# Optimization experiments

Measured on AMD Instinct MI355X. Metric: run time of the kernel, lower is better.

Reference implementation:

```python
import jax, jax.numpy as jnp
import numpy as np

D_C, D_K, D_T = 1024, 1024, 1024
N_KB = 65536
BATCH = 4096
ALPHA_C, ALPHA_K, ALPHA_T = 1.0, 0.5, 0.25


def setup_inputs() -> dict:
    key = jax.random.key(0)
    k1, k2, k3 = jax.random.split(key, 3)
    C = jax.random.normal(k1, (BATCH, D_C), dtype=jnp.float32)
    K = jax.random.normal(k2, (BATCH, D_K), dtype=jnp.float32)
    tie_kb = jax.random.normal(k3, (N_KB, D_T), dtype=jnp.float32)
    # Frozen Q: zero-initialized then identity on the top-left min(D_C, D_T) block.
    Q_weight = jnp.zeros((D_T, D_C), dtype=jnp.float32)
    d = min(D_C, D_T)
    Q_weight = Q_weight.at[:d, :d].set(jnp.eye(d, dtype=jnp.float32))
    return {
        "C": C,
        "K": K,
        "tie_kb": tie_kb,
        "Q_weight": Q_weight,
        "temperature": 1.0,
        "top_k": 32,
    }


def _retrieve_tie_batched(q, kb, top_k, temperature):
    """Batched version of the per-row retrieve_tie: cdist -> top-k nearest ->
    softmax(-dist/temperature) weighted sum of KB rows.
    q: [n, D_T], kb: [N_kb, D_T] -> [n, D_T]
    """
    q_sq = jnp.sum(q * q, axis=-1, keepdims=True)            # [n, 1]
    kb_sq = jnp.sum(kb * kb, axis=-1)                        # [N_kb]
    # Squared Euclidean distances via GEMM (same math as torch.cdist p=2)
    d2 = jnp.maximum(q_sq + kb_sq[None, :] - 2.0 * (q @ kb.T), 0.0)  # [n, N_kb]
    dist = jnp.sqrt(d2)
    neg_top, idx = jax.lax.top_k(-dist, top_k)               # top_k smallest dists
    w = jax.nn.softmax(neg_top / temperature, axis=-1)       # [n, top_k]
    sel = kb[idx]                                            # [n, top_k, D_T]
    return jnp.einsum('nk,nkd->nd', w, sel)


def reference(C, K, tie_kb, Q_weight, temperature, top_k):
    q = C @ Q_weight.T                                       # [n, D_T]
    T = _retrieve_tie_batched(q, tie_kb, top_k, temperature)  # [n, D_T]
    fused = jnp.concatenate([ALPHA_C * C, ALPHA_K * K, ALPHA_T * T], axis=1)
    return jax.nn.silu(fused)
```

## Files before the change

kernel.cpp:

```cpp
#include <hip/hip_runtime.h>
#include <stdint.h>

#define D_DIM   1024
#define NKB     65536
#define BATCH   4096
#define TOPK    32
#define NCHUNKS 16
#define CHUNK   4096
#define MT      128
#define NT      128
#define BKK     64
#define RB      16
#define RB_P    17

typedef float  floatx4 __attribute__((ext_vector_type(4)));
typedef __bf16 bf16x8  __attribute__((ext_vector_type(8)));

__device__ __forceinline__ uint16_t f2bf(float f) {
  union { float f; uint32_t i; } v; v.f = f;
  return (uint16_t)((v.i + 0x7fffu + ((v.i >> 16) & 1u)) >> 16);
}
__device__ __forceinline__ float silu_f(float x) { return x / (1.f + __expf(-x)); }

__device__ __forceinline__ void gl_lds16(const uint16_t* g, uint16_t* l) {
  __builtin_amdgcn_global_load_lds((const __attribute__((address_space(1))) void*)g,
                                   (__attribute__((address_space(3))) void*)l,
                                   16, 0, 0);
}

__global__ void convert_norms_kernel(const float* __restrict__ KB,
                                     const float* __restrict__ C,
                                     uint16_t* __restrict__ KBb,
                                     uint16_t* __restrict__ Cb,
                                     float* __restrict__ kbsq,
                                     float* __restrict__ qsq) {
  int wid  = (blockIdx.x * blockDim.x + threadIdx.x) >> 6;
  int lane = threadIdx.x & 63;
  if (wid >= NKB + BATCH) return;
  const float* src; uint16_t* dst;
  if (wid < NKB) { src = KB + (size_t)wid * D_DIM; dst = KBb + (size_t)wid * D_DIM; }
  else { src = C + (size_t)(wid - NKB) * D_DIM; dst = Cb + (size_t)(wid - NKB) * D_DIM; }

  const float4* p = (const float4*)src;
  uint4* q = (uint4*)dst;
  float s = 0.f;
  float4 f[4];
#pragma unroll
  for (int h = 0; h < 4; ++h) f[h] = p[lane * 4 + h];
  uint32_t ob[8];
#pragma unroll
  for (int h = 0; h < 4; ++h) {
    float vv[4] = {f[h].x, f[h].y, f[h].z, f[h].w};
#pragma unroll
    for (int e = 0; e < 4; ++e) s += vv[e] * vv[e];
    ob[h * 2]     = (uint32_t)f2bf(vv[0]) | ((uint32_t)f2bf(vv[1]) << 16);
    ob[h * 2 + 1] = (uint32_t)f2bf(vv[2]) | ((uint32_t)f2bf(vv[3]) << 16);
  }
  q[lane * 2]     = (uint4){ob[0], ob[1], ob[2], ob[3]};
  q[lane * 2 + 1] = (uint4){ob[4], ob[5], ob[6], ob[7]};
#pragma unroll
  for (int off = 32; off > 0; off >>= 1) s += __shfl_xor(s, off);
  if (lane == 0) { if (wid < NKB) kbsq[wid] = s; else qsq[wid - NKB] = s; }
}

__launch_bounds__(256, 2)
__global__ void dist_topk_kernel(const uint16_t* __restrict__ Cb,
                                 const uint16_t* __restrict__ KBb,
                                 const float* __restrict__ kbsq,
                                 const float* __restrict__ qsq,
                                 float* __restrict__ cand_d,
                                 int*   __restrict__ cand_i) {
  __shared__ __align__(16) uint16_t As[MT * BKK];
  __shared__ __align__(16) uint16_t Bs[NT * BKK];
  __shared__ float    rbd[MT * RB_P];
  __shared__ uint16_t rbi[MT * RB_P];
  __shared__ int      rbcnt[MT];
  __shared__ float    thr[MT];
  __shared__ float    qsq_l[MT];
  __shared__ int      s_any;

  const int t = threadIdx.x;
  const int w = t >> 6, lane = t & 63;
  const int lm = lane & 15, lq = lane >> 4;
  const int wr = w >> 1, wc = w & 1;
  const int row0 = blockIdx.x * MT;
  const int col0 = blockIdx.y * CHUNK;

  float tv[TOPK]; int ti[TOPK];
#pragma unroll
  for (int k = 0; k < TOPK; ++k) { tv[k] = __builtin_inff(); ti[k] = 0; }

  auto drain_rb = [&](int tt) {
    int n = rbcnt[tt]; if (n > RB) n = RB;
    for (int e = 0; e < n; ++e) {
      float d = rbd[tt * RB_P + e];
      int  iv = rbi[tt * RB_P + e];
      if (d < tv[TOPK - 1]) {
#pragma unroll
        for (int p = TOPK - 1; p >= 1; --p) {
          bool lt_prev = d < tv[p - 1];
          bool lt_here = d < tv[p];
          float nv = lt_prev ? tv[p - 1] : (lt_here ? d : tv[p]);
          int   ni = lt_prev ? ti[p - 1] : (lt_here ? iv : ti[p]);
          tv[p] = nv; ti[p] = ni;
        }
        if (d < tv[0]) { tv[0] = d; ti[0] = iv; }
      }
    }
    rbcnt[tt] = 0;
    thr[tt] = tv[TOPK - 1];
  };

  if (t < MT) { thr[t] = __builtin_inff(); rbcnt[t] = 0; qsq_l[t] = qsq[row0 + t]; }
  if (t == 0) s_any = 0;
  __syncthreads();

  bool pending = false;

  for (int ct = 0; ct < CHUNK / NT; ++ct) {
    const int cb = col0 + ct * NT;
    floatx4 acc[4][4];
#pragma unroll
    for (int i = 0; i < 4; ++i)
#pragma unroll
      for (int j = 0; j < 4; ++j) acc[i][j] = (floatx4){0.f, 0.f, 0.f, 0.f};

    for (int k0 = 0; k0 < D_DIM; k0 += BKK) {
      __syncthreads();
#pragma unroll
      for (int is = 0; is < 4; ++is) {
        int c = is * 256 + t;
        int row = c >> 3, kp = c & 7;
        int kps = kp ^ (row & 7);
        gl_lds16(Cb + (size_t)(row0 + row) * D_DIM + k0 + kps * 8,
                 &As[(is * 256 + (w << 6)) * 8]);
      }
#pragma unroll
      for (int is = 0; is < 4; ++is) {
        int c = is * 256 + t;
        int row = c >> 3, kp = c & 7;
        int kps = kp ^ (row & 7);
        gl_lds16(KBb + (size_t)(cb + row) * D_DIM + k0 + kps * 8,
                 &Bs[(is * 256 + (w << 6)) * 8]);
      }
      if (k0 == 0 && pending) {
        if (t < MT) drain_rb(t);
        pending = false;
      }
      __syncthreads();
#pragma unroll
      for (int kk = 0; kk < 2; ++kk) {
        bf16x8 af[4], bf[4];
#pragma unroll
        for (int i = 0; i < 4; ++i) {
          int r = (wr << 6) + (i << 4) + lm;
          int p = (kk * 4 + lq) ^ (r & 7);
          af[i] = *(const bf16x8*)&As[r * BKK + p * 8];
        }
#pragma unroll
        for (int j = 0; j < 4; ++j) {
          int r = (wc << 6) + (j << 4) + lm;
          int p = (kk * 4 + lq) ^ (r & 7);
          bf[j] = *(const bf16x8*)&Bs[r * BKK + p * 8];
        }
#pragma unroll
        for (int i = 0; i < 4; ++i)
#pragma unroll
          for (int j = 0; j < 4; ++j)
            acc[i][j] = __builtin_amdgcn_mfma_f32_16x16x32_bf16(af[i], bf[j], acc[i][j], 0, 0, 0);
      }
    }

    float kbc[4];
#pragma unroll
    for (int j = 0; j < 4; ++j) kbc[j] = kbsq[cb + (wc << 6) + (j << 4) + lm];

    uint64_t pend = 0;
#pragma unroll
    for (int i = 0; i < 4; ++i) {
#pragma unroll
      for (int rg = 0; rg < 4; ++rg) {
        int rl = (wr << 6) + (i << 4) + (lq << 2) + rg;
        float qv = qsq_l[rl];
        float th = thr[rl];
#pragma unroll
        for (int j = 0; j < 4; ++j) {
          float d2 = fmaf(-2.f, acc[i][j][rg], qv + kbc[j]);
          if (d2 < th) {
            int slot = atomicAdd(&rbcnt[rl], 1);
            if (slot < RB) {
              rbd[rl * RB_P + slot] = d2;
              rbi[rl * RB_P + slot] = (uint16_t)(cb + (wc << 6) + (j << 4) + lm);
            } else pend |= 1ull << ((i << 4) | (rg << 2) | j);
          }
        }
      }
    }
    if (pend) s_any = 1;
    __syncthreads();

    if (s_any) {
      while (true) {
        if (t < MT) drain_rb(t);
        if (t == 0) s_any = 0;
        __syncthreads();
        uint64_t np = 0;
#pragma unroll
        for (int i = 0; i < 4; ++i) {
#pragma unroll
          for (int rg = 0; rg < 4; ++rg) {
            int rl = (wr << 6) + (i << 4) + (lq << 2) + rg;
#pragma unroll
            for (int j = 0; j < 4; ++j) {
              const int v = (i << 4) | (rg << 2) | j;
              if (pend & (1ull << v)) {
                float d2 = fmaf(-2.f, acc[i][j][rg], qsq_l[rl] + kbc[j]);
                if (d2 < thr[rl]) {
                  int slot = atomicAdd(&rbcnt[rl], 1);
                  if (slot < RB) {
                    rbd[rl * RB_P + slot] = d2;
                    rbi[rl * RB_P + slot] = (uint16_t)(cb + (wc << 6) + (j << 4) + lm);
                  } else np |= 1ull << v;
                }
              }
            }
          }
        }
        pend = np;
        if (pend) s_any = 1;
        __syncthreads();
        if (!s_any) break;
      }
    } else {
      pending = true;
    }
  }

  if (pending) {
    if (t < MT) drain_rb(t);
  }

  if (t < MT) {
    size_t base = ((size_t)(row0 + t) * NCHUNKS + blockIdx.y) * TOPK;
#pragma unroll
    for (int k = 0; k < TOPK; ++k) {
      cand_d[base + k] = tv[k];
      cand_i[base + k] = ti[k];
    }
  }
}

__global__ void merge_kernel(const float* __restrict__ Cm,
                             const float* __restrict__ Km,
                             const float* __restrict__ KB,
                             const float* __restrict__ cand_d,
                             const int*   __restrict__ cand_i,
                             float* __restrict__ out) {
  __shared__ float sel_d[4][TOPK];
  __shared__ int   sel_i[4][TOPK];
  __shared__ float wgt[4][TOPK];
  int w = threadIdx.x >> 6, lane = threadIdx.x & 63;
  int R = blockIdx.x * 4 + w;

  float v[8]; int ix[8];
#pragma unroll
  for (int s = 0; s < 8; ++s) {
    v[s]  = cand_d[(size_t)R * (NCHUNKS * TOPK) + s * 64 + lane];
    ix[s] = cand_i[(size_t)R * (NCHUNKS * TOPK) + s * 64 + lane];
  }
  for (int k = 0; k < TOPK; ++k) {
    float bm = v[0]; int bs = 0;
#pragma unroll
    for (int s = 1; s < 8; ++s) if (v[s] < bm) { bm = v[s]; bs = s; }
    float m = bm; int ml = lane;
#pragma unroll
    for (int off = 32; off > 0; off >>= 1) {
      float om = __shfl_xor(m, off);
      int   ol = __shfl_xor(ml, off);
      if (om < m || (om == m && ol < ml)) { m = om; ml = ol; }
    }
    if (lane == ml) { sel_d[w][k] = bm; sel_i[w][k] = ix[bs]; v[bs] = __builtin_inff(); }
  }
  float dmin = sqrtf(fmaxf(sel_d[w][0], 0.f));
  float e = 0.f;
  if (lane < TOPK) e = __expf(dmin - sqrtf(fmaxf(sel_d[w][lane], 0.f)));
  float sum = e;
#pragma unroll
  for (int off = 32; off > 0; off >>= 1) sum += __shfl_xor(sum, off);
  if (lane < TOPK) wgt[w][lane] = e / sum;

  float accT[16];
#pragma unroll
  for (int s = 0; s < 16; ++s) accT[s] = 0.f;
  int d0 = lane * 16;
  for (int k = 0; k < TOPK; ++k) {
    int idx = sel_i[w][k] & 0xFFFF;
    float wk = wgt[w][k];
    const float4* kp = (const float4*)(KB + (size_t)idx * D_DIM + d0);
#pragma unroll
    for (int h = 0; h < 4; ++h) {
      float4 q = kp[h];
      accT[h * 4 + 0] = fmaf(wk, q.x, accT[h * 4 + 0]);
      accT[h * 4 + 1] = fmaf(wk, q.y, accT[h * 4 + 1]);
      accT[h * 4 + 2] = fmaf(wk, q.z, accT[h * 4 + 2]);
      accT[h * 4 + 3] = fmaf(wk, q.w, accT[h * 4 + 3]);
    }
  }

  size_t ob = (size_t)R * 3072;
  const float4* cp  = (const float4*)(Cm + (size_t)R * D_DIM + d0);
  const float4* kp2 = (const float4*)(Km + (size_t)R * D_DIM + d0);
#pragma unroll
  for (int h = 0; h < 4; ++h) {
    float4 c = cp[h], kq = kp2[h], o;
    o.x = silu_f(c.x); o.y = silu_f(c.y); o.z = silu_f(c.z); o.w = silu_f(c.w);
    ((float4*)&out[ob + d0])[h] = o;
    o.x = silu_f(0.5f * kq.x); o.y = silu_f(0.5f * kq.y);
    o.z = silu_f(0.5f * kq.z); o.w = silu_f(0.5f * kq.w);
    ((float4*)&out[ob + 1024 + d0])[h] = o;
    o.x = silu_f(0.25f * accT[h * 4 + 0]); o.y = silu_f(0.25f * accT[h * 4 + 1]);
    o.z = silu_f(0.25f * accT[h * 4 + 2]); o.w = silu_f(0.25f * accT[h * 4 + 3]);
    ((float4*)&out[ob + 2048 + d0])[h] = o;
  }
}

extern "C" void kernel_launch(void* const* d_in, const int* in_sizes, int n_in,
                              void* d_out, int out_size, void* d_ws, size_t ws_size,
                              hipStream_t stream) {
  (void)in_sizes; (void)n_in; (void)out_size; (void)ws_size;
  const float* Cm = (const float*)d_in[0];
  const float* Km = (const float*)d_in[1];
  const float* KB = (const float*)d_in[2];
  uint8_t* ws = (uint8_t*)d_ws;
  uint16_t* KBb  = (uint16_t*)ws;
  uint16_t* Cb   = (uint16_t*)(ws + 134217728);
  float*    kbsq = (float*)(ws + 134217728 + 8388608);
  float*    qsq  = (float*)(ws + 134217728 + 8388608 + 262144);
  float*    cand_d = (float*)(ws + 142884864);
  int*      cand_i = (int*)(ws + 142884864 + 8388608);
  float*    out  = (float*)d_out;

  convert_norms_kernel<<<dim3((NKB + BATCH) / 4), 256, 0, stream>>>(KB, Cm, KBb, Cb, kbsq, qsq);
  dist_topk_kernel<<<dim3(BATCH / MT, NCHUNKS), 256, 0, stream>>>(Cb, KBb, kbsq, qsq, cand_d, cand_i);
  merge_kernel<<<dim3(BATCH / 4), 256, 0, stream>>>(Cm, Km, KB, cand_d, cand_i, out);
}
```

Before: 1.660 ms.

## Double-buffer LDS tiles with async global-to-LDS prefetch and restructure buffer drain

Splits the A/B shared tiles into two buffers and issues the next k-slice's global_load_lds before computing the current one, waiting with explicit vmcnt counts and raw s_barrier. The first tile of the next column chunk is prefetched during the top-k filtering epilogue. The deferred drain of the candidate buffer, which used to overlap with the next chunk's loads, becomes an unconditional drain loop after every chunk. This doubles LDS for tiles, which may reduce occupancy, and adds extra barriers per chunk.

```diff
diff --git a/kernel.cpp b/kernel.cpp
--- a/kernel.cpp
+++ b/kernel.cpp
@@ -10,6 +10,7 @@
 #define MT      128
 #define NT      128
 #define BKK     64
+#define NK0     (D_DIM / BKK)
 #define RB      16
 #define RB_P    17
 
@@ -70,8 +71,8 @@
                                  const float* __restrict__ qsq,
                                  float* __restrict__ cand_d,
                                  int*   __restrict__ cand_i) {
-  __shared__ __align__(16) uint16_t As[MT * BKK];
-  __shared__ __align__(16) uint16_t Bs[NT * BKK];
+  __shared__ __align__(16) uint16_t As[2][MT * BKK];
+  __shared__ __align__(16) uint16_t Bs[2][NT * BKK];
   __shared__ float    rbd[MT * RB_P];
   __shared__ uint16_t rbi[MT * RB_P];
   __shared__ int      rbcnt[MT];
@@ -111,11 +112,30 @@
     thr[tt] = tv[TOPK - 1];
   };
 
+  auto stage = [&](int cbase, int k0, int buf) {
+#pragma unroll
+    for (int is = 0; is < 4; ++is) {
+      int c = is * 256 + t;
+      int row = c >> 3, kp = c & 7;
+      int kps = kp ^ (row & 7);
+      gl_lds16(Cb + (size_t)(row0 + row) * D_DIM + k0 + kps * 8,
+               &As[buf][(is * 256 + (w << 6)) * 8]);
+    }
+#pragma unroll
+    for (int is = 0; is < 4; ++is) {
+      int c = is * 256 + t;
+      int row = c >> 3, kp = c & 7;
+      int kps = kp ^ (row & 7);
+      gl_lds16(KBb + (size_t)(cbase + row) * D_DIM + k0 + kps * 8,
+               &Bs[buf][(is * 256 + (w << 6)) * 8]);
+    }
+  };
+
   if (t < MT) { thr[t] = __builtin_inff(); rbcnt[t] = 0; qsq_l[t] = qsq[row0 + t]; }
   if (t == 0) s_any = 0;
   __syncthreads();
 
-  bool pending = false;
+  stage(col0, 0, 0);
 
   for (int ct = 0; ct < CHUNK / NT; ++ct) {
     const int cb = col0 + ct * NT;
@@ -125,29 +145,19 @@
 #pragma unroll
       for (int j = 0; j < 4; ++j) acc[i][j] = (floatx4){0.f, 0.f, 0.f, 0.f};
 
-    for (int k0 = 0; k0 < D_DIM; k0 += BKK) {
-      __syncthreads();
-#pragma unroll
-      for (int is = 0; is < 4; ++is) {
-        int c = is * 256 + t;
-        int row = c >> 3, kp = c & 7;
-        int kps = kp ^ (row & 7);
-        gl_lds16(Cb + (size_t)(row0 + row) * D_DIM + k0 + kps * 8,
-                 &As[(is * 256 + (w << 6)) * 8]);
-      }
-#pragma unroll
-      for (int is = 0; is < 4; ++is) {
-        int c = is * 256 + t;
-        int row = c >> 3, kp = c & 7;
-        int kps = kp ^ (row & 7);
-        gl_lds16(KBb + (size_t)(cb + row) * D_DIM + k0 + kps * 8,
-                 &Bs[(is * 256 + (w << 6)) * 8]);
-      }
-      if (k0 == 0 && pending) {
-        if (t < MT) drain_rb(t);
-        pending = false;
-      }
-      __syncthreads();
+    for (int k0s = 0; k0s < NK0; ++k0s) {
+      const int cur = k0s & 1;
+      if (k0s < NK0 - 1) {
+        stage(cb, (k0s + 1) * BKK, cur ^ 1);
+        __builtin_amdgcn_sched_barrier(0);
+        asm volatile("s_waitcnt vmcnt(8)" ::: "memory");
+      } else {
+        __builtin_amdgcn_sched_barrier(0);
+        asm volatile("s_waitcnt vmcnt(0)" ::: "memory");
+      }
+      __builtin_amdgcn_sched_barrier(0);
+      __builtin_amdgcn_s_barrier();
+      __builtin_amdgcn_sched_barrier(0);
 #pragma unroll
       for (int kk = 0; kk < 2; ++kk) {
         bf16x8 af[4], bf[4];
@@ -155,13 +165,13 @@
         for (int i = 0; i < 4; ++i) {
           int r = (wr << 6) + (i << 4) + lm;
           int p = (kk * 4 + lq) ^ (r & 7);
-          af[i] = *(const bf16x8*)&As[r * BKK + p * 8];
+          af[i] = *(const bf16x8*)&As[cur][r * BKK + p * 8];
         }
 #pragma unroll
         for (int j = 0; j < 4; ++j) {
           int r = (wc << 6) + (j << 4) + lm;
           int p = (kk * 4 + lq) ^ (r & 7);
-          bf[j] = *(const bf16x8*)&Bs[r * BKK + p * 8];
+          bf[j] = *(const bf16x8*)&Bs[cur][r * BKK + p * 8];
         }
 #pragma unroll
         for (int i = 0; i < 4; ++i)
@@ -169,7 +179,12 @@
           for (int j = 0; j < 4; ++j)
             acc[i][j] = __builtin_amdgcn_mfma_f32_16x16x32_bf16(af[i], bf[j], acc[i][j], 0, 0, 0);
       }
-    }
+      __builtin_amdgcn_sched_barrier(0);
+      __builtin_amdgcn_s_barrier();
+      __builtin_amdgcn_sched_barrier(0);
+    }
+
+    if (ct + 1 < CHUNK / NT) stage(cb + NT, 0, 0);
 
     float kbc[4];
 #pragma unroll
@@ -196,48 +211,41 @@
         }
       }
     }
-    if (pend) s_any = 1;
     __syncthreads();
 
-    if (s_any) {
-      while (true) {
-        if (t < MT) drain_rb(t);
-        if (t == 0) s_any = 0;
-        __syncthreads();
-        uint64_t np = 0;
-#pragma unroll
-        for (int i = 0; i < 4; ++i) {
-#pragma unroll
-          for (int rg = 0; rg < 4; ++rg) {
-            int rl = (wr << 6) + (i << 4) + (lq << 2) + rg;
-#pragma unroll
-            for (int j = 0; j < 4; ++j) {
-              const int v = (i << 4) | (rg << 2) | j;
-              if (pend & (1ull << v)) {
-                float d2 = fmaf(-2.f, acc[i][j][rg], qsq_l[rl] + kbc[j]);
-                if (d2 < thr[rl]) {
-                  int slot = atomicAdd(&rbcnt[rl], 1);
-                  if (slot < RB) {
-                    rbd[rl * RB_P + slot] = d2;
-                    rbi[rl * RB_P + slot] = (uint16_t)(cb + (wc << 6) + (j << 4) + lm);
-                  } else np |= 1ull << v;
-                }
+    while (true) {
+      if (t < MT) drain_rb(t);
+      __syncthreads();
+      if (pend) s_any = 1;
+      __syncthreads();
+      if (!s_any) break;
+      uint64_t np = 0;
+#pragma unroll
+      for (int i = 0; i < 4; ++i) {
+#pragma unroll
+        for (int rg = 0; rg < 4; ++rg) {
+          int rl = (wr << 6) + (i << 4) + (lq << 2) + rg;
+#pragma unroll
+          for (int j = 0; j < 4; ++j) {
+            const int v = (i << 4) | (rg << 2) | j;
+            if (pend & (1ull << v)) {
+              float d2 = fmaf(-2.f, acc[i][j][rg], qsq_l[rl] + kbc[j]);
+              if (d2 < thr[rl]) {
+                int slot = atomicAdd(&rbcnt[rl], 1);
+                if (slot < RB) {
+                  rbd[rl * RB_P + slot] = d2;
+                  rbi[rl * RB_P + slot] = (uint16_t)(cb + (wc << 6) + (j << 4) + lm);
+                } else np |= 1ull << v;
               }
             }
           }
         }
-        pend = np;
-        if (pend) s_any = 1;
-        __syncthreads();
-        if (!s_any) break;
-      }
-    } else {
-      pending = true;
-    }
-  }
-
-  if (pending) {
-    if (t < MT) drain_rb(t);
+      }
+      pend = np;
+      __syncthreads();
+      if (t == 0) s_any = 0;
+      __syncthreads();
+    }
   }
 
   if (t < MT) {
```

Result: no change. 1.672 ms (+0.8%).
